# Optimization experiments

Hardware: AMD Instinct MI355X
Metric: run time of the kernel (lower is better)

## Reference

```python
import jax, jax.numpy as jnp
import numpy as np

BLOCK_SIZES = [256] * 16
LAYER_SIZE = sum(BLOCK_SIZES)  # 4096
N_ROWS = 8192


def _block_diag_mask(sizes):
    m = np.zeros((sum(sizes), sum(sizes)), dtype=bool)
    off = 0
    for s in sizes:
        m[off:off + s, off:off + s] = True
        off += s
    return jnp.asarray(m)


def setup_inputs() -> dict:
    key = jax.random.key(0)
    k1, k2 = jax.random.split(key)
    mask = _block_diag_mask(BLOCK_SIZES)
    # _blocks param: block_diagonal(raw_blocks) -> dense matrix, zero off-block
    blocks = jax.random.normal(k1, (LAYER_SIZE, LAYER_SIZE), dtype=jnp.float32) * mask
    x = jax.random.normal(k2, (N_ROWS, LAYER_SIZE), dtype=jnp.float32)
    return {"x": x, "blocks": blocks, "mask": mask}


def reference(x, blocks, mask):
    # blocks property: mask then tanh (constrained='tanh'); tanh(0)=0 preserves structure
    b = jnp.tanh(blocks * mask)
    # forward: dense matmul x @ blocks (no bias)
    return x @ b
```

## Files before the change

kernel.cpp:

```cpp
#include <hip/hip_runtime.h>
#include <stdint.h>


typedef float floatx4 __attribute__((ext_vector_type(4)));
typedef __bf16 bf16x8 __attribute__((ext_vector_type(8)));

#define LDX 4096
#define NBLK 16
#define BS 256
#define BM 64
#define BN 256
#define BK 32

__device__ __forceinline__ unsigned int f2bf(float f) {
  union { float f; unsigned int i; } x;
  x.f = f;
  unsigned int r = x.i + 0x7FFFu + ((x.i >> 16) & 1u);
  return r >> 16;
}

__device__ __forceinline__ void async_copy16(const void* g, void* l) {
  __builtin_amdgcn_global_load_lds(
      (__attribute__((address_space(1))) void*)(uintptr_t)g,
      (__attribute__((address_space(3))) void*)(unsigned int)(uintptr_t)l,
      16, 0, 0);
}

__global__ __launch_bounds__(256) void tanh_pack(const float* __restrict__ blocks,
                                                 unsigned short* __restrict__ wsT) {
  __shared__ float tile[64][65];
  const int t = threadIdx.x;
  const int tc = blockIdx.x, tr = blockIdx.y, j = blockIdx.z;
  const float* src = blocks + (size_t)(j * BS + tr * 64) * LDX + j * BS + tc * 64;
#pragma unroll
  for (int it = 0; it < 8; ++it) {
    int v = it * 256 + t;
    int row = v >> 5;
    int c2 = (v & 31) * 2;
    float2 f = *(const float2*)(src + (size_t)row * LDX + c2);
    tile[row][c2] = tanhf(f.x);
    tile[row][c2 + 1] = tanhf(f.y);
  }
  __syncthreads();
  unsigned short* dst = wsT + (size_t)j * BS * BS + (size_t)(tc * 64) * BS + tr * 64;
#pragma unroll
  for (int it = 0; it < 8; ++it) {
    int v = it * 256 + t;
    int nn = v >> 5;
    int k2 = (v & 31) * 2;
    unsigned int pair = f2bf(tile[k2][nn]) | (f2bf(tile[k2 + 1][nn]) << 16);
    *(unsigned int*)(dst + (size_t)nn * BS + k2) = pair;
  }
}

template <int BSTR, bool FUSED>
__global__ __launch_bounds__(256) void bdgemm(const float* __restrict__ x,
                                              const void* __restrict__ bsrc,
                                              float* __restrict__ out) {
  __shared__ unsigned short As[BM * BK];
  __shared__ unsigned short Bs[BN * BSTR];
  const int t = threadIdx.x;
  const int lane = t & 63;
  const int wave = t >> 6;
  const int mtile = blockIdx.x;
  const int j = blockIdx.y;
  const int m0 = mtile * BM;

  const float* xg = x + (size_t)m0 * LDX + j * BS;

  const int srow = t >> 2;
  const int scol = (t & 3) * 8;
  const int wn = wave * 64;
  const int fr = lane & 15;
  const int fq = (lane >> 4) * 8;

  floatx4 acc[4][4];
#pragma unroll
  for (int a = 0; a < 4; ++a)
#pragma unroll
    for (int b = 0; b < 4; ++b) acc[a][b] = (floatx4){0.f, 0.f, 0.f, 0.f};

  for (int kt = 0; kt < 8; ++kt) {
    const int k0 = kt * BK;
    const float* ap = xg + (size_t)srow * LDX + k0 + scol;
    float4 a0 = *(const float4*)(ap);
    float4 a1 = *(const float4*)(ap + 4);
    uint4 pk;
    pk.x = f2bf(a0.x) | (f2bf(a0.y) << 16);
    pk.y = f2bf(a0.z) | (f2bf(a0.w) << 16);
    pk.z = f2bf(a1.x) | (f2bf(a1.y) << 16);
    pk.w = f2bf(a1.z) | (f2bf(a1.w) << 16);
    *(uint4*)(As + t * 8) = pk;

    if constexpr (!FUSED) {
      const unsigned short* wsb =
          (const unsigned short*)bsrc + (size_t)j * BS * BS;
#pragma unroll
      for (int i = 0; i < 4; ++i) {
        const int n = i * 64 + (t >> 2);
        async_copy16(wsb + (size_t)n * BS + k0 + scol, Bs + i * 2048 + t * 8);
      }
    } else {
      const float* bg = (const float*)bsrc;
#pragma unroll
      for (int i = 0; i < 32; ++i) {
        const int idx = i * 256 + t;
        const int kk = idx >> 8;
        const int nn = idx & 255;
        float v = tanhf(bg[(size_t)(j * BS + k0 + kk) * LDX + j * BS + nn]);
        Bs[nn * BSTR + kk] = (unsigned short)f2bf(v);
      }
    }
    __syncthreads();

    bf16x8 af[4], bfm[4];
#pragma unroll
    for (int i = 0; i < 4; ++i) {
      af[i] = *(const bf16x8*)(As + (i * 16 + fr) * BK + fq);
      bfm[i] = *(const bf16x8*)(Bs + (wn + i * 16 + fr) * BSTR + fq);
    }
#pragma unroll
    for (int mi = 0; mi < 4; ++mi)
#pragma unroll
      for (int ni = 0; ni < 4; ++ni)
        acc[mi][ni] =
            __builtin_amdgcn_mfma_f32_16x16x32_bf16(af[mi], bfm[ni], acc[mi][ni], 0, 0, 0);
    __syncthreads();
  }

  const int r0 = (lane >> 4) * 4;
  const int ocol = j * BS + wn + fr;
#pragma unroll
  for (int mi = 0; mi < 4; ++mi)
#pragma unroll
    for (int ni = 0; ni < 4; ++ni) {
      float* op = out + (size_t)(m0 + mi * 16 + r0) * LDX + ocol + ni * 16;
#pragma unroll
      for (int r = 0; r < 4; ++r) op[(size_t)r * LDX] = acc[mi][ni][r];
    }
}

extern "C" void kernel_launch(void* const* d_in, const int* in_sizes, int n_in,
                              void* d_out, int out_size, void* d_ws, size_t ws_size,
                              hipStream_t stream) {
  const float* x = (const float*)d_in[0];
  const float* blocks = (const float*)d_in[1];
  float* out = (float*)d_out;

  const size_t need = (size_t)NBLK * BS * BS * sizeof(unsigned short);
  dim3 grid(128, NBLK);
  if (d_ws != nullptr && ws_size >= need) {
    unsigned short* wsT = (unsigned short*)d_ws;
    tanh_pack<<<dim3(4, 4, NBLK), 256, 0, stream>>>(blocks, wsT);
    bdgemm<BK, false><<<grid, 256, 0, stream>>>(x, wsT, out);
  } else {
    bdgemm<40, true><<<grid, 256, 0, stream>>>(x, blocks, out);
  }
}
```

Before: 318.3 us.

## Keep weight fragments in registers and stream x rows directly into MFMA

Replaces the LDS-tiled block GEMM with a kernel where each wave preloads its 256x64 bf16 weight slice into registers once, then streams 16-row slabs of x from global memory directly into MFMA operands. This removes LDS staging and per-k-step barriers, and launches fewer, longer-lived blocks. In exchange it uses many VGPRs, which limits occupancy, and each x row is loaded redundantly by four waves, relying on cache.

```diff
diff --git a/kernel.cpp b/kernel.cpp
--- a/kernel.cpp
+++ b/kernel.cpp
@@ -8,9 +8,9 @@
 #define LDX 4096
 #define NBLK 16
 #define BS 256
-#define BM 64
-#define BN 256
-#define BK 32
+#define WPJ 32
+#define MSTEPS 16
+#define MROWS 16
 
 __device__ __forceinline__ unsigned int f2bf(float f) {
   union { float f; unsigned int i; } x;
@@ -19,11 +19,13 @@
   return r >> 16;
 }
 
-__device__ __forceinline__ void async_copy16(const void* g, void* l) {
-  __builtin_amdgcn_global_load_lds(
-      (__attribute__((address_space(1))) void*)(uintptr_t)g,
-      (__attribute__((address_space(3))) void*)(unsigned int)(uintptr_t)l,
-      16, 0, 0);
+__device__ __forceinline__ bf16x8 cvt8(float4 a, float4 b) {
+  union { unsigned int u[4]; bf16x8 v; } r;
+  r.u[0] = f2bf(a.x) | (f2bf(a.y) << 16);
+  r.u[1] = f2bf(a.z) | (f2bf(a.w) << 16);
+  r.u[2] = f2bf(b.x) | (f2bf(b.y) << 16);
+  r.u[3] = f2bf(b.z) | (f2bf(b.w) << 16);
+  return r.v;
 }
 
 __global__ __launch_bounds__(256) void tanh_pack(const float* __restrict__ blocks,
@@ -53,21 +55,67 @@
   }
 }
 
-template <int BSTR, bool FUSED>
-__global__ __launch_bounds__(256) void bdgemm(const float* __restrict__ x,
-                                              const void* __restrict__ bsrc,
-                                              float* __restrict__ out) {
-  __shared__ unsigned short As[BM * BK];
-  __shared__ unsigned short Bs[BN * BSTR];
+__global__ __launch_bounds__(256, 2) void bdgemm_stream(const float* __restrict__ x,
+                                                        const unsigned short* __restrict__ wsT,
+                                                        float* __restrict__ out) {
+  const int t = threadIdx.x;
+  const int lane = t & 63;
+  const int wave = t >> 6;
+  const int mslab = blockIdx.x;
+  const int j = blockIdx.y;
+  const int fr = lane & 15;
+  const int fq = (lane >> 4) * 8;
+  const int n0w = wave * 64;
+  const int r0 = (lane >> 4) * 4;
+
+  const unsigned short* wb = wsT + (size_t)j * (BS * BS);
+  bf16x8 Bf[8][4];
+#pragma unroll
+  for (int kw = 0; kw < 8; ++kw)
+#pragma unroll
+    for (int nf = 0; nf < 4; ++nf)
+      Bf[kw][nf] = *(const bf16x8*)(wb + (size_t)(n0w + nf * 16 + fr) * BS + kw * 32 + fq);
+
+  const int col0 = j * BS + n0w + fr;
+  for (int step = 0; step < MSTEPS; ++step) {
+    const int m0 = (mslab * MSTEPS + step) * MROWS;
+    const float* ax = x + (size_t)(m0 + fr) * LDX + j * BS + fq;
+
+    floatx4 acc[4];
+#pragma unroll
+    for (int nf = 0; nf < 4; ++nf) acc[nf] = (floatx4){0.f, 0.f, 0.f, 0.f};
+
+#pragma unroll
+    for (int kw = 0; kw < 8; ++kw) {
+      float4 f0 = *(const float4*)(ax + kw * 32);
+      float4 f1 = *(const float4*)(ax + kw * 32 + 4);
+      bf16x8 av = cvt8(f0, f1);
+#pragma unroll
+      for (int nf = 0; nf < 4; ++nf)
+        acc[nf] = __builtin_amdgcn_mfma_f32_16x16x32_bf16(av, Bf[kw][nf], acc[nf], 0, 0, 0);
+    }
+
+#pragma unroll
+    for (int nf = 0; nf < 4; ++nf) {
+      float* op = out + (size_t)(m0 + r0) * LDX + col0 + nf * 16;
+#pragma unroll
+      for (int r = 0; r < 4; ++r) op[(size_t)r * LDX] = acc[nf][r];
+    }
+  }
+}
+
+__global__ __launch_bounds__(256) void bdgemm_fused(const float* __restrict__ x,
+                                                    const float* __restrict__ blocks,
+                                                    float* __restrict__ out) {
+  __shared__ unsigned short As[64 * 32];
+  __shared__ unsigned short Bs[256 * 40];
   const int t = threadIdx.x;
   const int lane = t & 63;
   const int wave = t >> 6;
   const int mtile = blockIdx.x;
   const int j = blockIdx.y;
-  const int m0 = mtile * BM;
-
+  const int m0 = mtile * 64;
   const float* xg = x + (size_t)m0 * LDX + j * BS;
-
   const int srow = t >> 2;
   const int scol = (t & 3) * 8;
   const int wn = wave * 64;
@@ -81,7 +129,7 @@
     for (int b = 0; b < 4; ++b) acc[a][b] = (floatx4){0.f, 0.f, 0.f, 0.f};
 
   for (int kt = 0; kt < 8; ++kt) {
-    const int k0 = kt * BK;
+    const int k0 = kt * 32;
     const float* ap = xg + (size_t)srow * LDX + k0 + scol;
     float4 a0 = *(const float4*)(ap);
     float4 a1 = *(const float4*)(ap + 4);
@@ -91,33 +139,20 @@
     pk.z = f2bf(a1.x) | (f2bf(a1.y) << 16);
     pk.w = f2bf(a1.z) | (f2bf(a1.w) << 16);
     *(uint4*)(As + t * 8) = pk;
-
-    if constexpr (!FUSED) {
-      const unsigned short* wsb =
-          (const unsigned short*)bsrc + (size_t)j * BS * BS;
 #pragma unroll
-      for (int i = 0; i < 4; ++i) {
-        const int n = i * 64 + (t >> 2);
-        async_copy16(wsb + (size_t)n * BS + k0 + scol, Bs + i * 2048 + t * 8);
-      }
-    } else {
-      const float* bg = (const float*)bsrc;
-#pragma unroll
-      for (int i = 0; i < 32; ++i) {
-        const int idx = i * 256 + t;
-        const int kk = idx >> 8;
-        const int nn = idx & 255;
-        float v = tanhf(bg[(size_t)(j * BS + k0 + kk) * LDX + j * BS + nn]);
-        Bs[nn * BSTR + kk] = (unsigned short)f2bf(v);
-      }
+    for (int i = 0; i < 32; ++i) {
+      const int idx = i * 256 + t;
+      const int kk = idx >> 8;
+      const int nn = idx & 255;
+      float v = tanhf(blocks[(size_t)(j * BS + k0 + kk) * LDX + j * BS + nn]);
+      Bs[nn * 40 + kk] = (unsigned short)f2bf(v);
     }
     __syncthreads();
-
     bf16x8 af[4], bfm[4];
 #pragma unroll
     for (int i = 0; i < 4; ++i) {
-      af[i] = *(const bf16x8*)(As + (i * 16 + fr) * BK + fq);
-      bfm[i] = *(const bf16x8*)(Bs + (wn + i * 16 + fr) * BSTR + fq);
+      af[i] = *(const bf16x8*)(As + (i * 16 + fr) * 32 + fq);
+      bfm[i] = *(const bf16x8*)(Bs + (wn + i * 16 + fr) * 40 + fq);
     }
 #pragma unroll
     for (int mi = 0; mi < 4; ++mi)
@@ -127,7 +162,6 @@
             __builtin_amdgcn_mfma_f32_16x16x32_bf16(af[mi], bfm[ni], acc[mi][ni], 0, 0, 0);
     __syncthreads();
   }
-
   const int r0 = (lane >> 4) * 4;
   const int ocol = j * BS + wn + fr;
 #pragma unroll
@@ -148,12 +182,11 @@
   float* out = (float*)d_out;
 
   const size_t need = (size_t)NBLK * BS * BS * sizeof(unsigned short);
-  dim3 grid(128, NBLK);
   if (d_ws != nullptr && ws_size >= need) {
     unsigned short* wsT = (unsigned short*)d_ws;
     tanh_pack<<<dim3(4, 4, NBLK), 256, 0, stream>>>(blocks, wsT);
-    bdgemm<BK, false><<<grid, 256, 0, stream>>>(x, wsT, out);
+    bdgemm_stream<<<dim3(WPJ, NBLK), 256, 0, stream>>>(x, wsT, out);
   } else {
-    bdgemm<40, true><<<grid, 256, 0, stream>>>(x, blocks, out);
+    bdgemm_fused<<<dim3(128, NBLK), 256, 0, stream>>>(x, blocks, out);
   }
 }
```

Result: slower. 357.5 us (+12.3%).
